# Kernel optimization log

Measured on AMD Instinct MI355X. Metric: run time of the kernel, lower is better.

The kernel has to match this reference:

```python
import jax, jax.numpy as jnp
import numpy as np

DIM = 1024
N_HEAD = 16
HEAD_DIM = DIM // N_HEAD
SCALE = HEAD_DIM ** (-0.5)


def setup_inputs() -> dict:
    key = jax.random.key(0)
    ks = jax.random.split(key, 5)
    x = jax.random.normal(ks[0], (2, 2048, DIM), dtype=jnp.float32)
    # Linear params (torch nn.Linear stores weight as [out, in]; we keep [in, out])
    wqkv = jax.random.normal(ks[1], (DIM, 3 * DIM), dtype=jnp.float32) / np.sqrt(DIM)
    bqkv = jax.random.normal(ks[2], (3 * DIM,), dtype=jnp.float32) * 0.01
    wo = jax.random.normal(ks[3], (DIM, DIM), dtype=jnp.float32) / np.sqrt(DIM)
    bo = jax.random.normal(ks[4], (DIM,), dtype=jnp.float32) * 0.01
    return {"x": x, "wqkv": wqkv, "bqkv": bqkv, "wo": wo, "bo": bo}


def reference(x, wqkv, bqkv, wo, bo):
    b, s, _ = x.shape
    qkv = x @ wqkv + bqkv                      # [b, s, 3*dim]
    q, k, v = jnp.split(qkv, 3, axis=-1)
    # [b, s, h, d] -> [b, h, s, d]
    def heads(t):
        return t.reshape(b, s, N_HEAD, HEAD_DIM).transpose(0, 2, 1, 3)
    q, k, v = heads(q) * SCALE, heads(k), heads(v)
    attn = jnp.einsum('bhqd,bhkd->bhqk', q, k)  # [b, h, s, s]
    attn = jax.nn.softmax(attn, axis=-1)
    out = jnp.einsum('bhqk,bhkd->bhqd', attn, v)
    out = out.transpose(0, 2, 1, 3).reshape(b, s, DIM)
    return out @ wo + bo
```

## Files before the change

### kernel.cpp

```cpp
#include <hip/hip_runtime.h>
#include <hip/hip_bf16.h>

#define DIM   1024
#define NHEAD 16
#define HDIM  64
#define BATCH 2
#define SEQ   2048
#define TOK   (BATCH*SEQ)
#define QSCALE 0.1803368801111204f

typedef unsigned short u16;
typedef __attribute__((ext_vector_type(8))) _Float16 h16x8;
typedef __attribute__((ext_vector_type(2))) __fp16 fp16x2;
typedef __attribute__((ext_vector_type(4))) float f32x4;
typedef __attribute__((ext_vector_type(16))) float f32x16;
typedef __attribute__((ext_vector_type(2))) int i32x2;

__device__ __forceinline__ u16 f2h(float f) {
    union { _Float16 h; u16 u; } v; v.h = (_Float16)f;
    return v.u;
}
__device__ __forceinline__ unsigned pack2h(float a, float b) {
    return (unsigned)f2h(a) | ((unsigned)f2h(b) << 16);
}
__device__ __forceinline__ unsigned pkrtz(float a, float b) {
    union { fp16x2 h; unsigned u; } v;
    v.h = __builtin_amdgcn_cvt_pkrtz(a, b);
    return v.u;
}
__device__ __forceinline__ f32x16 zero16() {
    f32x16 v;
#pragma unroll
    for (int i = 0; i < 16; ++i) v[i] = 0.f;
    return v;
}

typedef __attribute__((address_space(3))) void lds_void;
typedef const __attribute__((address_space(1))) void gbl_void;
__device__ __forceinline__ void gload_lds16(const void* g, void* l) {
    __builtin_amdgcn_global_load_lds((gbl_void*)g, (lds_void*)l, 16, 0, 0);
}

__global__ __launch_bounds__(256)
void cvt_f16(const float* __restrict__ in, u16* __restrict__ out) {
    int i = blockIdx.x * 256 + threadIdx.x;
    float4 v = ((const float4*)in)[i];
    ((uint2*)out)[i] = make_uint2(pack2h(v.x, v.y), pack2h(v.z, v.w));
}

__global__ __launch_bounds__(256)
void cvt_f16_T(const float* __restrict__ in, u16* __restrict__ outT,
               int K, int N) {
    __shared__ float t[32][33];
    const int n0 = blockIdx.x * 32, k0 = blockIdx.y * 32;
    const int tx = threadIdx.x & 31, ty = threadIdx.x >> 5;
#pragma unroll
    for (int i = 0; i < 4; ++i)
        t[ty + i * 8][tx] = in[(size_t)(k0 + ty + i * 8) * N + n0 + tx];
    __syncthreads();
#pragma unroll
    for (int i = 0; i < 4; ++i)
        outT[(size_t)(n0 + ty + i * 8) * K + k0 + tx] = f2h(t[tx][ty + i * 8]);
}

__global__ __launch_bounds__(256)
void gemm_qkv(const u16* __restrict__ Ag, const u16* __restrict__ Bg,
              const float* __restrict__ bias, u16* __restrict__ Qh,
              u16* __restrict__ Kh, u16* __restrict__ Vh, int K, int N) {
    __shared__ u16 As[128 * 64];
    __shared__ u16 Bs[128 * 64];

    const int tid  = threadIdx.x;
    const int lane = tid & 63;
    const int w    = tid >> 6;
    const int c    = lane & 15;
    const int quad = lane >> 4;
    const int wm   = (w & 1) * 64;
    const int wn   = (w >> 1) * 64;
    const int row0 = blockIdx.y * 128;
    const int col0 = blockIdx.x * 128;
    const int sw   = c & 7;

    f32x4 acc[4][4];
#pragma unroll
    for (int m = 0; m < 4; ++m)
#pragma unroll
        for (int n = 0; n < 4; ++n) acc[m][n] = (f32x4){0.f, 0.f, 0.f, 0.f};

    for (int k0 = 0; k0 < K; k0 += 64) {
        __syncthreads();
#pragma unroll
        for (int i = 0; i < 4; ++i) {
            int idx = tid + i * 256;
            int r = idx >> 3, p = idx & 7;
            int g = p ^ (r & 7);
            gload_lds16(Ag + (size_t)(row0 + r) * K + k0 + g * 8, &As[idx * 8]);
            gload_lds16(Bg + (size_t)(col0 + r) * K + k0 + g * 8, &Bs[idx * 8]);
        }
        __syncthreads();

        h16x8 af[4][2];
#pragma unroll
        for (int m = 0; m < 4; ++m)
#pragma unroll
            for (int kh = 0; kh < 2; ++kh)
                af[m][kh] = *(const h16x8*)&As[(wm + m * 16 + c) * 64 +
                                              ((kh * 4 + quad) ^ sw) * 8];
#pragma unroll
        for (int kh = 0; kh < 2; ++kh)
#pragma unroll
            for (int n = 0; n < 4; ++n) {
                h16x8 bf = *(const h16x8*)&Bs[(wn + n * 16 + c) * 64 +
                                              ((kh * 4 + quad) ^ sw) * 8];
#pragma unroll
                for (int m = 0; m < 4; ++m)
                    acc[m][n] = __builtin_amdgcn_mfma_f32_16x16x32_f16(
                        af[m][kh], bf, acc[m][n], 0, 0, 0);
            }
    }

#pragma unroll
    for (int n = 0; n < 4; ++n) {
        const int col = col0 + wn + n * 16 + c;
        const float bv = bias[col];
        const int h = (col >> 6) & 15, d = col & 63;
#pragma unroll
        for (int m = 0; m < 4; ++m) {
            const int rbase = row0 + wm + m * 16 + quad * 4;
            const int b = rbase >> 11, s0 = rbase & (SEQ - 1);
            const int bh = (b << 4) + h;
            if (col0 < DIM) {
#pragma unroll
                for (int r = 0; r < 4; ++r)
                    Qh[((size_t)bh * SEQ + s0 + r) * 64 + d] =
                        f2h((acc[m][n][r] + bv) * QSCALE);
            } else if (col0 < 2 * DIM) {
#pragma unroll
                for (int r = 0; r < 4; ++r)
                    Kh[((size_t)bh * SEQ + s0 + r) * 64 + d] =
                        f2h(acc[m][n][r] + bv);
            } else {
                uint2 pv = make_uint2(pack2h(acc[m][n][0] + bv, acc[m][n][1] + bv),
                                      pack2h(acc[m][n][2] + bv, acc[m][n][3] + bv));
                *(uint2*)&Vh[((size_t)bh * 64 + d) * SEQ + s0] = pv;
            }
        }
    }
}

__global__ __launch_bounds__(256)
void gemm_out(const u16* __restrict__ Ag, const u16* __restrict__ Bg,
              const float* __restrict__ bias, float* __restrict__ Cout,
              int M, int N, int K) {
    __shared__ u16 As[128 * 64];
    __shared__ u16 Bs[64 * 64];

    const int tid  = threadIdx.x;
    const int lane = tid & 63;
    const int w    = tid >> 6;
    const int c    = lane & 15;
    const int quad = lane >> 4;
    const int wm   = w * 32;
    const int row0 = blockIdx.y * 128;
    const int col0 = blockIdx.x * 64;
    const int sw   = c & 7;

    f32x4 acc[2][4];
#pragma unroll
    for (int m = 0; m < 2; ++m)
#pragma unroll
        for (int n = 0; n < 4; ++n) acc[m][n] = (f32x4){0.f, 0.f, 0.f, 0.f};

    for (int k0 = 0; k0 < K; k0 += 64) {
        __syncthreads();
#pragma unroll
        for (int i = 0; i < 4; ++i) {
            int idx = tid + i * 256;
            int r = idx >> 3, p = idx & 7;
            int g = p ^ (r & 7);
            gload_lds16(Ag + (size_t)(row0 + r) * K + k0 + g * 8, &As[idx * 8]);
        }
#pragma unroll
        for (int i = 0; i < 2; ++i) {
            int idx = tid + i * 256;
            int r = idx >> 3, p = idx & 7;
            int g = p ^ (r & 7);
            gload_lds16(Bg + (size_t)(col0 + r) * K + k0 + g * 8, &Bs[idx * 8]);
        }
        __syncthreads();

        h16x8 af[2][2];
#pragma unroll
        for (int m = 0; m < 2; ++m)
#pragma unroll
            for (int kh = 0; kh < 2; ++kh)
                af[m][kh] = *(const h16x8*)&As[(wm + m * 16 + c) * 64 +
                                              ((kh * 4 + quad) ^ sw) * 8];
#pragma unroll
        for (int kh = 0; kh < 2; ++kh)
#pragma unroll
            for (int n = 0; n < 4; ++n) {
                h16x8 bf = *(const h16x8*)&Bs[(n * 16 + c) * 64 +
                                              ((kh * 4 + quad) ^ sw) * 8];
#pragma unroll
                for (int m = 0; m < 2; ++m)
                    acc[m][n] = __builtin_amdgcn_mfma_f32_16x16x32_f16(
                        af[m][kh], bf, acc[m][n], 0, 0, 0);
            }
    }

#pragma unroll
    for (int n = 0; n < 4; ++n) {
        const int col = col0 + n * 16 + c;
        const float bv = bias[col];
#pragma unroll
        for (int m = 0; m < 2; ++m) {
            const int rbase = row0 + wm + m * 16 + quad * 4;
#pragma unroll
            for (int r = 0; r < 4; ++r)
                Cout[(size_t)(rbase + r) * N + col] = acc[m][n][r] + bv;
        }
    }
}

__global__ __launch_bounds__(256, 2)
void flash_attn11(const u16* __restrict__ Qg, const u16* __restrict__ Kg,
                  const u16* __restrict__ Vg, u16* __restrict__ aout) {
    __shared__ u16 Qs[128 * 64];
    __shared__ u16 Ks[2][128 * 64];
    __shared__ u16 Vt[2][64 * 128];

    const int tid  = threadIdx.x;
    const int lane = tid & 63;
    const int w    = tid >> 6;
    const int wq   = w & 1;
    const int wk   = w >> 1;
    const int n32  = lane & 31;
    const int q5   = lane >> 5;
    const int bh   = blockIdx.y;
    const int q0   = blockIdx.x * 128;

    const u16* Qb = Qg + (size_t)bh * SEQ * 64;
    const u16* Kb = Kg + (size_t)bh * SEQ * 64;
    const u16* Vb = Vg + (size_t)bh * 64 * SEQ;

#pragma unroll
    for (int i = 0; i < 4; ++i) {
        int idx = tid + i * 256;
        int r = idx >> 3, p = idx & 7, g = p ^ (r & 7);
        gload_lds16(Qb + (size_t)(q0 + r) * 64 + g * 8, &Qs[idx * 8]);
    }
#pragma unroll
    for (int i = 0; i < 4; ++i) {
        int idx = tid + i * 256;
        int rk = idx >> 3, pk = idx & 7, gk = pk ^ (rk & 7);
        gload_lds16(Kb + (size_t)rk * 64 + gk * 8, &Ks[0][idx * 8]);
        int rv = idx >> 4, cv = idx & 15, gv = cv ^ (rv & 7);
        gload_lds16(Vb + (size_t)rv * SEQ + gv * 8, &Vt[0][idx * 8]);
    }
    __syncthreads();

    const int qrowA = wq * 64 + n32;
    const int qrowB = qrowA + 32;
    const int sw    = n32 & 7;
    h16x8 qbA[4], qbB[4];
#pragma unroll
    for (int s = 0; s < 4; ++s) {
        const int ch = ((s * 2 + q5) ^ sw) * 8;
        qbA[s] = *(const h16x8*)&Qs[qrowA * 64 + ch];
        qbB[s] = *(const h16x8*)&Qs[qrowB * 64 + ch];
    }

    float lA = 0.f, lB = 0.f;
    f32x16 oA[2] = {zero16(), zero16()};
    f32x16 oB[2] = {zero16(), zero16()};

    for (int kt = 0; kt < SEQ / 128; ++kt) {
        const int cur = kt & 1, nxt = cur ^ 1;

        if (kt < SEQ / 128 - 1) {
            const int k1 = (kt + 1) * 128;
#pragma unroll
            for (int i = 0; i < 4; ++i) {
                int idx = tid + i * 256;
                int rk = idx >> 3, pk = idx & 7, gk = pk ^ (rk & 7);
                gload_lds16(Kb + (size_t)(k1 + rk) * 64 + gk * 8, &Ks[nxt][idx * 8]);
                int rv = idx >> 4, cv = idx & 15, gv = cv ^ (rv & 7);
                gload_lds16(Vb + (size_t)rv * SEQ + k1 + gv * 8, &Vt[nxt][idx * 8]);
            }
        }

        unsigned xwA[8][2], xwB[8][2];
#pragma unroll
        for (int sub = 0; sub < 2; ++sub) {
            const int kr = wk * 64 + sub * 32 + n32;
            f32x16 saA = zero16(), saB = zero16();
            __builtin_amdgcn_s_setprio(1);
#pragma unroll
            for (int s = 0; s < 4; ++s) {
                h16x8 ak = *(const h16x8*)&Ks[cur][kr * 64 +
                                                   (((s * 2 + q5) ^ sw) * 8)];
                saA = __builtin_amdgcn_mfma_f32_32x32x16_f16(ak, qbA[s], saA, 0, 0, 0);
                saB = __builtin_amdgcn_mfma_f32_32x32x16_f16(ak, qbB[s], saB, 0, 0, 0);
            }
            __builtin_amdgcn_s_setprio(0);
#pragma unroll
            for (int rr = 0; rr < 4; ++rr) {
                float a0 = __builtin_amdgcn_exp2f(saA[4 * rr + 0]);
                float a1 = __builtin_amdgcn_exp2f(saA[4 * rr + 1]);
                float a2 = __builtin_amdgcn_exp2f(saA[4 * rr + 2]);
                float a3 = __builtin_amdgcn_exp2f(saA[4 * rr + 3]);
                lA += (a0 + a1) + (a2 + a3);
                xwA[sub * 4 + rr][0] = pkrtz(a0, a1);
                xwA[sub * 4 + rr][1] = pkrtz(a2, a3);
                float b0 = __builtin_amdgcn_exp2f(saB[4 * rr + 0]);
                float b1 = __builtin_amdgcn_exp2f(saB[4 * rr + 1]);
                float b2 = __builtin_amdgcn_exp2f(saB[4 * rr + 2]);
                float b3 = __builtin_amdgcn_exp2f(saB[4 * rr + 3]);
                lB += (b0 + b1) + (b2 + b3);
                xwB[sub * 4 + rr][0] = pkrtz(b0, b1);
                xwB[sub * 4 + rr][1] = pkrtz(b2, b3);
            }
        }

        h16x8 bpA[4], bpB[4];
#pragma unroll
        for (int s = 0; s < 4; ++s) {
            i32x2 ra = __builtin_amdgcn_permlane32_swap(
                (int)xwA[2 * s][0], (int)xwA[2 * s + 1][0], false, false);
            i32x2 rb = __builtin_amdgcn_permlane32_swap(
                (int)xwA[2 * s][1], (int)xwA[2 * s + 1][1], false, false);
            union { int u[4]; h16x8 h; } fa;
            fa.u[0] = ra[0]; fa.u[1] = rb[0]; fa.u[2] = ra[1]; fa.u[3] = rb[1];
            bpA[s] = fa.h;
            i32x2 rc = __builtin_amdgcn_permlane32_swap(
                (int)xwB[2 * s][0], (int)xwB[2 * s + 1][0], false, false);
            i32x2 rd = __builtin_amdgcn_permlane32_swap(
                (int)xwB[2 * s][1], (int)xwB[2 * s + 1][1], false, false);
            union { int u[4]; h16x8 h; } fb;
            fb.u[0] = rc[0]; fb.u[1] = rd[0]; fb.u[2] = rc[1]; fb.u[3] = rd[1];
            bpB[s] = fb.h;
        }

        __builtin_amdgcn_s_setprio(1);
#pragma unroll
        for (int dt = 0; dt < 2; ++dt) {
            const int dr = dt * 32 + n32;
#pragma unroll
            for (int s = 0; s < 4; ++s) {
                h16x8 av = *(const h16x8*)&Vt[cur][dr * 128 +
                                                   ((wk * 8 + ((s * 2 + q5) ^ sw)) * 8)];
                oA[dt] = __builtin_amdgcn_mfma_f32_32x32x16_f16(av, bpA[s], oA[dt], 0, 0, 0);
                oB[dt] = __builtin_amdgcn_mfma_f32_32x32x16_f16(av, bpB[s], oB[dt], 0, 0, 0);
            }
        }
        __builtin_amdgcn_s_setprio(0);

        __syncthreads();
    }

    lA += __shfl_xor(lA, 32, 64);
    lB += __shfl_xor(lB, 32, 64);

    float* oc = (float*)Vt;
    float* lc = (float*)Qs;
    const int rowA = (wq * 2 + 0) * 64 + lane;
    const int rowB = (wq * 2 + 1) * 64 + lane;
    if (wk == 1) {
#pragma unroll
        for (int dt = 0; dt < 2; ++dt)
#pragma unroll
            for (int i = 0; i < 16; ++i) {
                oc[rowA * 32 + ((dt * 16 + i + lane) & 31)] = oA[dt][i];
                oc[rowB * 32 + ((dt * 16 + i + lane) & 31)] = oB[dt][i];
            }
        lc[rowA] = lA;
        lc[rowB] = lB;
    }
    __syncthreads();
    if (wk == 1) return;
    lA += lc[rowA];
    lB += lc[rowB];
#pragma unroll
    for (int dt = 0; dt < 2; ++dt)
#pragma unroll
        for (int i = 0; i < 16; ++i) {
            oA[dt][i] += oc[rowA * 32 + ((dt * 16 + i + lane) & 31)];
            oB[dt][i] += oc[rowB * 32 + ((dt * 16 + i + lane) & 31)];
        }

    const float invA = 1.f / lA, invB = 1.f / lB;
    const int b = bh >> 4, h = bh & 15;
    const size_t roA = (size_t)(b * SEQ + q0 + qrowA) * DIM + h * HDIM;
    const size_t roB = (size_t)(b * SEQ + q0 + qrowB) * DIM + h * HDIM;
#pragma unroll
    for (int dt = 0; dt < 2; ++dt) {
#pragma unroll
        for (int rq = 0; rq < 4; ++rq) {
            const int d = dt * 32 + 8 * rq + 4 * q5;
            *(uint2*)&aout[roA + d] = make_uint2(
                pkrtz(oA[dt][4 * rq + 0] * invA, oA[dt][4 * rq + 1] * invA),
                pkrtz(oA[dt][4 * rq + 2] * invA, oA[dt][4 * rq + 3] * invA));
            *(uint2*)&aout[roB + d] = make_uint2(
                pkrtz(oB[dt][4 * rq + 0] * invB, oB[dt][4 * rq + 1] * invB),
                pkrtz(oB[dt][4 * rq + 2] * invB, oB[dt][4 * rq + 3] * invB));
        }
    }
}

extern "C" void kernel_launch(void* const* d_in, const int* in_sizes, int n_in,
                              void* d_out, int out_size, void* d_ws, size_t ws_size,
                              hipStream_t stream) {
    (void)in_sizes; (void)n_in; (void)out_size; (void)ws_size;
    const float* x    = (const float*)d_in[0];
    const float* wqkv = (const float*)d_in[1];
    const float* bqkv = (const float*)d_in[2];
    const float* wo   = (const float*)d_in[3];
    const float* bo   = (const float*)d_in[4];
    float* out = (float*)d_out;

    const size_t HB = (size_t)BATCH * NHEAD * SEQ * HDIM;
    u16* Qh  = (u16*)d_ws;
    u16* Kh  = Qh + HB;
    u16* Vh  = Kh + HB;
    u16* ao  = Vh + HB;
    u16* wqT = ao + (size_t)TOK * DIM;
    u16* woT = wqT + (size_t)3 * DIM * DIM;
    u16* xh  = woT + (size_t)DIM * DIM;

    cvt_f16<<<TOK * DIM / 4 / 256, 256, 0, stream>>>(x, xh);
    cvt_f16_T<<<dim3(3 * DIM / 32, DIM / 32), 256, 0, stream>>>(wqkv, wqT, DIM, 3 * DIM);
    cvt_f16_T<<<dim3(DIM / 32, DIM / 32), 256, 0, stream>>>(wo, woT, DIM, DIM);
    gemm_qkv<<<dim3(3 * DIM / 128, TOK / 128), 256, 0, stream>>>(
        xh, wqT, bqkv, Qh, Kh, Vh, DIM, 3 * DIM);
    flash_attn11<<<dim3(SEQ / 128, BATCH * NHEAD), 256, 0, stream>>>(
        Qh, Kh, Vh, ao);
    gemm_out<<<dim3(DIM / 64, TOK / 128), 256, 0, stream>>>(
        ao, woT, bo, out, TOK, DIM, DIM);
}
```

Measured before the change: 184.8 us.

## Load attention Q/K/V fragments directly from global into registers, drop LDS staging

The attention kernel stops staging Q, K and V tiles in shared memory with double-buffered async copies and block barriers. Each wave now loads its MFMA operand fragments straight from global memory into registers, software-pipelining K one tile ahead, while V is loaded at the start of each iteration. This removes the per-tile __syncthreads and the LDS traffic, but each pair of waves now fetches the same K/V data separately through cache, and uses more registers and longer exposed global latency.

```diff
diff --git a/kernel.cpp b/kernel.cpp
--- a/kernel.cpp
+++ b/kernel.cpp
@@ -224,11 +224,10 @@
 }
 
 __global__ __launch_bounds__(256, 2)
-void flash_attn11(const u16* __restrict__ Qg, const u16* __restrict__ Kg,
+void flash_attn12(const u16* __restrict__ Qg, const u16* __restrict__ Kg,
                   const u16* __restrict__ Vg, u16* __restrict__ aout) {
-    __shared__ u16 Qs[128 * 64];
-    __shared__ u16 Ks[2][128 * 64];
-    __shared__ u16 Vt[2][64 * 128];
+    __shared__ float oc[256 * 32];
+    __shared__ float lc[256];
 
     const int tid  = threadIdx.x;
     const int lane = tid & 63;
@@ -244,64 +243,71 @@
     const u16* Kb = Kg + (size_t)bh * SEQ * 64;
     const u16* Vb = Vg + (size_t)bh * 64 * SEQ;
 
-#pragma unroll
-    for (int i = 0; i < 4; ++i) {
-        int idx = tid + i * 256;
-        int r = idx >> 3, p = idx & 7, g = p ^ (r & 7);
-        gload_lds16(Qb + (size_t)(q0 + r) * 64 + g * 8, &Qs[idx * 8]);
-    }
-#pragma unroll
-    for (int i = 0; i < 4; ++i) {
-        int idx = tid + i * 256;
-        int rk = idx >> 3, pk = idx & 7, gk = pk ^ (rk & 7);
-        gload_lds16(Kb + (size_t)rk * 64 + gk * 8, &Ks[0][idx * 8]);
-        int rv = idx >> 4, cv = idx & 15, gv = cv ^ (rv & 7);
-        gload_lds16(Vb + (size_t)rv * SEQ + gv * 8, &Vt[0][idx * 8]);
-    }
-    __syncthreads();
-
     const int qrowA = wq * 64 + n32;
     const int qrowB = qrowA + 32;
-    const int sw    = n32 & 7;
+    const int ch0 = (0 + q5) * 8, ch1 = (2 + q5) * 8,
+              ch2 = (4 + q5) * 8, ch3 = (6 + q5) * 8;
+
     h16x8 qbA[4], qbB[4];
-#pragma unroll
-    for (int s = 0; s < 4; ++s) {
-        const int ch = ((s * 2 + q5) ^ sw) * 8;
-        qbA[s] = *(const h16x8*)&Qs[qrowA * 64 + ch];
-        qbB[s] = *(const h16x8*)&Qs[qrowB * 64 + ch];
+    {
+        const u16* qa = Qb + (size_t)(q0 + qrowA) * 64;
+        const u16* qb_ = Qb + (size_t)(q0 + qrowB) * 64;
+        qbA[0] = *(const h16x8*)&qa[ch0];  qbA[1] = *(const h16x8*)&qa[ch1];
+        qbA[2] = *(const h16x8*)&qa[ch2];  qbA[3] = *(const h16x8*)&qa[ch3];
+        qbB[0] = *(const h16x8*)&qb_[ch0]; qbB[1] = *(const h16x8*)&qb_[ch1];
+        qbB[2] = *(const h16x8*)&qb_[ch2]; qbB[3] = *(const h16x8*)&qb_[ch3];
     }
 
     float lA = 0.f, lB = 0.f;
     f32x16 oA[2] = {zero16(), zero16()};
     f32x16 oB[2] = {zero16(), zero16()};
 
-    for (int kt = 0; kt < SEQ / 128; ++kt) {
-        const int cur = kt & 1, nxt = cur ^ 1;
-
-        if (kt < SEQ / 128 - 1) {
-            const int k1 = (kt + 1) * 128;
-#pragma unroll
-            for (int i = 0; i < 4; ++i) {
-                int idx = tid + i * 256;
-                int rk = idx >> 3, pk = idx & 7, gk = pk ^ (rk & 7);
-                gload_lds16(Kb + (size_t)(k1 + rk) * 64 + gk * 8, &Ks[nxt][idx * 8]);
-                int rv = idx >> 4, cv = idx & 15, gv = cv ^ (rv & 7);
-                gload_lds16(Vb + (size_t)rv * SEQ + k1 + gv * 8, &Vt[nxt][idx * 8]);
-            }
+    h16x8 kf0[2][4], kf1[2][4];
+    const u16* kr0 = Kb + (size_t)(wk * 64 + n32) * 64;
+    const u16* kr1 = Kb + (size_t)(wk * 64 + 32 + n32) * 64;
+    const u16* vr0 = Vb + (size_t)n32 * SEQ + wk * 64;
+    const u16* vr1 = Vb + (size_t)(32 + n32) * SEQ + wk * 64;
+
+#define LOAD_K(DST, OFF)                                                     \
+    {                                                                        \
+        DST[0][0] = *(const h16x8*)&kr0[(OFF) + ch0];                        \
+        DST[0][1] = *(const h16x8*)&kr0[(OFF) + ch1];                        \
+        DST[0][2] = *(const h16x8*)&kr0[(OFF) + ch2];                        \
+        DST[0][3] = *(const h16x8*)&kr0[(OFF) + ch3];                        \
+        DST[1][0] = *(const h16x8*)&kr1[(OFF) + ch0];                        \
+        DST[1][1] = *(const h16x8*)&kr1[(OFF) + ch1];                        \
+        DST[1][2] = *(const h16x8*)&kr1[(OFF) + ch2];                        \
+        DST[1][3] = *(const h16x8*)&kr1[(OFF) + ch3];                        \
+    }
+
+    LOAD_K(kf0, 0);
+
+    auto iter = [&](h16x8 (&KF)[2][4], h16x8 (&KN)[2][4], int T) {
+        if (T + 1 < SEQ / 128)
+            LOAD_K(KN, (size_t)(T + 1) * 128 * 64);
+
+        h16x8 vf[2][4];
+        {
+            const size_t vo = (size_t)T * 128;
+            vf[0][0] = *(const h16x8*)&vr0[vo + ch0];
+            vf[0][1] = *(const h16x8*)&vr0[vo + ch1];
+            vf[0][2] = *(const h16x8*)&vr0[vo + ch2];
+            vf[0][3] = *(const h16x8*)&vr0[vo + ch3];
+            vf[1][0] = *(const h16x8*)&vr1[vo + ch0];
+            vf[1][1] = *(const h16x8*)&vr1[vo + ch1];
+            vf[1][2] = *(const h16x8*)&vr1[vo + ch2];
+            vf[1][3] = *(const h16x8*)&vr1[vo + ch3];
         }
 
         unsigned xwA[8][2], xwB[8][2];
 #pragma unroll
         for (int sub = 0; sub < 2; ++sub) {
-            const int kr = wk * 64 + sub * 32 + n32;
             f32x16 saA = zero16(), saB = zero16();
             __builtin_amdgcn_s_setprio(1);
 #pragma unroll
             for (int s = 0; s < 4; ++s) {
-                h16x8 ak = *(const h16x8*)&Ks[cur][kr * 64 +
-                                                   (((s * 2 + q5) ^ sw) * 8)];
-                saA = __builtin_amdgcn_mfma_f32_32x32x16_f16(ak, qbA[s], saA, 0, 0, 0);
-                saB = __builtin_amdgcn_mfma_f32_32x32x16_f16(ak, qbB[s], saB, 0, 0, 0);
+                saA = __builtin_amdgcn_mfma_f32_32x32x16_f16(KF[sub][s], qbA[s], saA, 0, 0, 0);
+                saB = __builtin_amdgcn_mfma_f32_32x32x16_f16(KF[sub][s], qbB[s], saB, 0, 0, 0);
             }
             __builtin_amdgcn_s_setprio(0);
 #pragma unroll
@@ -344,26 +350,24 @@
 
         __builtin_amdgcn_s_setprio(1);
 #pragma unroll
-        for (int dt = 0; dt < 2; ++dt) {
-            const int dr = dt * 32 + n32;
+        for (int dt = 0; dt < 2; ++dt)
 #pragma unroll
             for (int s = 0; s < 4; ++s) {
-                h16x8 av = *(const h16x8*)&Vt[cur][dr * 128 +
-                                                   ((wk * 8 + ((s * 2 + q5) ^ sw)) * 8)];
-                oA[dt] = __builtin_amdgcn_mfma_f32_32x32x16_f16(av, bpA[s], oA[dt], 0, 0, 0);
-                oB[dt] = __builtin_amdgcn_mfma_f32_32x32x16_f16(av, bpB[s], oB[dt], 0, 0, 0);
-            }
-        }
+                oA[dt] = __builtin_amdgcn_mfma_f32_32x32x16_f16(vf[dt][s], bpA[s], oA[dt], 0, 0, 0);
+                oB[dt] = __builtin_amdgcn_mfma_f32_32x32x16_f16(vf[dt][s], bpB[s], oB[dt], 0, 0, 0);
+            }
         __builtin_amdgcn_s_setprio(0);
-
-        __syncthreads();
-    }
+    };
+
+    for (int kt = 0; kt < SEQ / 128; kt += 2) {
+        iter(kf0, kf1, kt);
+        iter(kf1, kf0, kt + 1);
+    }
+#undef LOAD_K
 
     lA += __shfl_xor(lA, 32, 64);
     lB += __shfl_xor(lB, 32, 64);
 
-    float* oc = (float*)Vt;
-    float* lc = (float*)Qs;
     const int rowA = (wq * 2 + 0) * 64 + lane;
     const int rowB = (wq * 2 + 1) * 64 + lane;
     if (wk == 1) {
@@ -433,7 +437,7 @@
     cvt_f16_T<<<dim3(DIM / 32, DIM / 32), 256, 0, stream>>>(wo, woT, DIM, DIM);
     gemm_qkv<<<dim3(3 * DIM / 128, TOK / 128), 256, 0, stream>>>(
         xh, wqT, bqkv, Qh, Kh, Vh, DIM, 3 * DIM);
-    flash_attn11<<<dim3(SEQ / 128, BATCH * NHEAD), 256, 0, stream>>>(
+    flash_attn12<<<dim3(SEQ / 128, BATCH * NHEAD), 256, 0, stream>>>(
         Qh, Kh, Vh, ao);
     gemm_out<<<dim3(DIM / 64, TOK / 128), 256, 0, stream>>>(
         ao, woT, bo, out, TOK, DIM, DIM);
```

Result: slower. 249.8 us (+35.2%).

## Double-buffer LDS in both GEMMs and enlarge out-projection tile to 128x128

Applied to the files above, without the earlier changes.

Both projection GEMMs now stage the next K-slice into a second LDS buffer while computing on the current one, which removes one barrier per iteration and overlaps the global-to-LDS loads with MFMA work. The output GEMM also moves from a 128x64 tile to 128x128 with a 2x2 warp layout, giving more reuse per block but half as many blocks (256) on the GPU. Shared memory per block doubles to 64KB, which may lower occupancy. Correctness depends on the async LDS loads being complete at the end-of-iteration barrier.

```diff
diff --git a/kernel.cpp b/kernel.cpp
--- a/kernel.cpp
+++ b/kernel.cpp
@@ -67,8 +67,8 @@
 void gemm_qkv(const u16* __restrict__ Ag, const u16* __restrict__ Bg,
               const float* __restrict__ bias, u16* __restrict__ Qh,
               u16* __restrict__ Kh, u16* __restrict__ Vh, int K, int N) {
-    __shared__ u16 As[128 * 64];
-    __shared__ u16 Bs[128 * 64];
+    __shared__ u16 As[2][128 * 64];
+    __shared__ u16 Bs[2][128 * 64];
 
     const int tid  = threadIdx.x;
     const int lane = tid & 63;
@@ -81,42 +81,50 @@
     const int col0 = blockIdx.x * 128;
     const int sw   = c & 7;
 
-    f32x4 acc[4][4];
-#pragma unroll
-    for (int m = 0; m < 4; ++m)
-#pragma unroll
-        for (int n = 0; n < 4; ++n) acc[m][n] = (f32x4){0.f, 0.f, 0.f, 0.f};
-
-    for (int k0 = 0; k0 < K; k0 += 64) {
-        __syncthreads();
+    auto stage = [&](int buf, int koff) {
 #pragma unroll
         for (int i = 0; i < 4; ++i) {
             int idx = tid + i * 256;
             int r = idx >> 3, p = idx & 7;
             int g = p ^ (r & 7);
-            gload_lds16(Ag + (size_t)(row0 + r) * K + k0 + g * 8, &As[idx * 8]);
-            gload_lds16(Bg + (size_t)(col0 + r) * K + k0 + g * 8, &Bs[idx * 8]);
-        }
-        __syncthreads();
+            gload_lds16(Ag + (size_t)(row0 + r) * K + koff + g * 8, &As[buf][idx * 8]);
+            gload_lds16(Bg + (size_t)(col0 + r) * K + koff + g * 8, &Bs[buf][idx * 8]);
+        }
+    };
+
+    f32x4 acc[4][4];
+#pragma unroll
+    for (int m = 0; m < 4; ++m)
+#pragma unroll
+        for (int n = 0; n < 4; ++n) acc[m][n] = (f32x4){0.f, 0.f, 0.f, 0.f};
+
+    stage(0, 0);
+    __syncthreads();
+    int cur = 0;
+    for (int k0 = 0; k0 < K; k0 += 64) {
+        if (k0 + 64 < K) stage(cur ^ 1, k0 + 64);
 
         h16x8 af[4][2];
 #pragma unroll
         for (int m = 0; m < 4; ++m)
 #pragma unroll
             for (int kh = 0; kh < 2; ++kh)
-                af[m][kh] = *(const h16x8*)&As[(wm + m * 16 + c) * 64 +
-                                              ((kh * 4 + quad) ^ sw) * 8];
+                af[m][kh] = *(const h16x8*)&As[cur][(wm + m * 16 + c) * 64 +
+                                                   ((kh * 4 + quad) ^ sw) * 8];
 #pragma unroll
         for (int kh = 0; kh < 2; ++kh)
 #pragma unroll
             for (int n = 0; n < 4; ++n) {
-                h16x8 bf = *(const h16x8*)&Bs[(wn + n * 16 + c) * 64 +
-                                              ((kh * 4 + quad) ^ sw) * 8];
+                h16x8 bf = *(const h16x8*)&Bs[cur][(wn + n * 16 + c) * 64 +
+                                                   ((kh * 4 + quad) ^ sw) * 8];
 #pragma unroll
                 for (int m = 0; m < 4; ++m)
                     acc[m][n] = __builtin_amdgcn_mfma_f32_16x16x32_f16(
                         af[m][kh], bf, acc[m][n], 0, 0, 0);
             }
+
+        __syncthreads();
+        cur ^= 1;
     }
 
 #pragma unroll
@@ -152,69 +160,72 @@
 void gemm_out(const u16* __restrict__ Ag, const u16* __restrict__ Bg,
               const float* __restrict__ bias, float* __restrict__ Cout,
               int M, int N, int K) {
-    __shared__ u16 As[128 * 64];
-    __shared__ u16 Bs[64 * 64];
+    __shared__ u16 As[2][128 * 64];
+    __shared__ u16 Bs[2][128 * 64];
 
     const int tid  = threadIdx.x;
     const int lane = tid & 63;
     const int w    = tid >> 6;
     const int c    = lane & 15;
     const int quad = lane >> 4;
-    const int wm   = w * 32;
+    const int wm   = (w & 1) * 64;
+    const int wn   = (w >> 1) * 64;
     const int row0 = blockIdx.y * 128;
-    const int col0 = blockIdx.x * 64;
+    const int col0 = blockIdx.x * 128;
     const int sw   = c & 7;
 
-    f32x4 acc[2][4];
-#pragma unroll
-    for (int m = 0; m < 2; ++m)
-#pragma unroll
-        for (int n = 0; n < 4; ++n) acc[m][n] = (f32x4){0.f, 0.f, 0.f, 0.f};
-
-    for (int k0 = 0; k0 < K; k0 += 64) {
-        __syncthreads();
+    auto stage = [&](int buf, int koff) {
 #pragma unroll
         for (int i = 0; i < 4; ++i) {
             int idx = tid + i * 256;
             int r = idx >> 3, p = idx & 7;
             int g = p ^ (r & 7);
-            gload_lds16(Ag + (size_t)(row0 + r) * K + k0 + g * 8, &As[idx * 8]);
-        }
-#pragma unroll
-        for (int i = 0; i < 2; ++i) {
-            int idx = tid + i * 256;
-            int r = idx >> 3, p = idx & 7;
-            int g = p ^ (r & 7);
-            gload_lds16(Bg + (size_t)(col0 + r) * K + k0 + g * 8, &Bs[idx * 8]);
-        }
-        __syncthreads();
-
-        h16x8 af[2][2];
-#pragma unroll
-        for (int m = 0; m < 2; ++m)
+            gload_lds16(Ag + (size_t)(row0 + r) * K + koff + g * 8, &As[buf][idx * 8]);
+            gload_lds16(Bg + (size_t)(col0 + r) * K + koff + g * 8, &Bs[buf][idx * 8]);
+        }
+    };
+
+    f32x4 acc[4][4];
+#pragma unroll
+    for (int m = 0; m < 4; ++m)
+#pragma unroll
+        for (int n = 0; n < 4; ++n) acc[m][n] = (f32x4){0.f, 0.f, 0.f, 0.f};
+
+    stage(0, 0);
+    __syncthreads();
+    int cur = 0;
+    for (int k0 = 0; k0 < K; k0 += 64) {
+        if (k0 + 64 < K) stage(cur ^ 1, k0 + 64);
+
+        h16x8 af[4][2];
+#pragma unroll
+        for (int m = 0; m < 4; ++m)
 #pragma unroll
             for (int kh = 0; kh < 2; ++kh)
-                af[m][kh] = *(const h16x8*)&As[(wm + m * 16 + c) * 64 +
-                                              ((kh * 4 + quad) ^ sw) * 8];
+                af[m][kh] = *(const h16x8*)&As[cur][(wm + m * 16 + c) * 64 +
+                                                   ((kh * 4 + quad) ^ sw) * 8];
 #pragma unroll
         for (int kh = 0; kh < 2; ++kh)
 #pragma unroll
             for (int n = 0; n < 4; ++n) {
-                h16x8 bf = *(const h16x8*)&Bs[(n * 16 + c) * 64 +
-                                              ((kh * 4 + quad) ^ sw) * 8];
-#pragma unroll
-                for (int m = 0; m < 2; ++m)
+                h16x8 bf = *(const h16x8*)&Bs[cur][(wn + n * 16 + c) * 64 +
+                                                   ((kh * 4 + quad) ^ sw) * 8];
+#pragma unroll
+                for (int m = 0; m < 4; ++m)
                     acc[m][n] = __builtin_amdgcn_mfma_f32_16x16x32_f16(
                         af[m][kh], bf, acc[m][n], 0, 0, 0);
             }
+
+        __syncthreads();
+        cur ^= 1;
     }
 
 #pragma unroll
     for (int n = 0; n < 4; ++n) {
-        const int col = col0 + n * 16 + c;
+        const int col = col0 + wn + n * 16 + c;
         const float bv = bias[col];
 #pragma unroll
-        for (int m = 0; m < 2; ++m) {
+        for (int m = 0; m < 4; ++m) {
             const int rbase = row0 + wm + m * 16 + quad * 4;
 #pragma unroll
             for (int r = 0; r < 4; ++r)
@@ -435,6 +446,6 @@
         xh, wqT, bqkv, Qh, Kh, Vh, DIM, 3 * DIM);
     flash_attn11<<<dim3(SEQ / 128, BATCH * NHEAD), 256, 0, stream>>>(
         Qh, Kh, Vh, ao);
-    gemm_out<<<dim3(DIM / 64, TOK / 128), 256, 0, stream>>>(
+    gemm_out<<<dim3(DIM / 128, TOK / 128), 256, 0, stream>>>(
         ao, woT, bo, out, TOK, DIM, DIM);
 }
```

Measured after the change: 190.9 us. 1.03x slower.

## Fuse conversion kernels into one launch and enlarge output GEMM tile to 128x128

Applied to the files above, without the earlier changes.

Merges the x fp16 conversion and the two weight transpose-conversion kernels into one launch, choosing the branch from the block index. This removes two kernel launches and the gaps between them. Also widens the output projection GEMM tile from 128x64 to 128x128, with each wave computing a 64x64 sub-tile, which gives more operand reuse per LDS load. The cost is that the output grid halves to 256 blocks and each thread keeps more accumulator registers, which can lower occupancy.

```diff
diff --git a/kernel.cpp b/kernel.cpp
--- a/kernel.cpp
+++ b/kernel.cpp
@@ -42,17 +42,22 @@
 }
 
 __global__ __launch_bounds__(256)
-void cvt_f16(const float* __restrict__ in, u16* __restrict__ out) {
-    int i = blockIdx.x * 256 + threadIdx.x;
-    float4 v = ((const float4*)in)[i];
-    ((uint2*)out)[i] = make_uint2(pack2h(v.x, v.y), pack2h(v.z, v.w));
-}
-
-__global__ __launch_bounds__(256)
-void cvt_f16_T(const float* __restrict__ in, u16* __restrict__ outT,
-               int K, int N) {
+void fused_cvt(const float* __restrict__ x,    u16* __restrict__ xh,
+               const float* __restrict__ wqkv, u16* __restrict__ wqT,
+               const float* __restrict__ wo,   u16* __restrict__ woT) {
     __shared__ float t[32][33];
-    const int n0 = blockIdx.x * 32, k0 = blockIdx.y * 32;
+    const int bid = blockIdx.x;
+    if (bid < 4096) {
+        int i = bid * 256 + threadIdx.x;
+        float4 v = ((const float4*)x)[i];
+        ((uint2*)xh)[i] = make_uint2(pack2h(v.x, v.y), pack2h(v.z, v.w));
+        return;
+    }
+    const float* in; u16* outT; int K, N, tb;
+    if (bid < 7168) { in = wqkv; outT = wqT; K = 1024; N = 3072; tb = bid - 4096; }
+    else            { in = wo;   outT = woT; K = 1024; N = 1024; tb = bid - 7168; }
+    const int nbx = N / 32;
+    const int n0 = (tb % nbx) * 32, k0 = (tb / nbx) * 32;
     const int tx = threadIdx.x & 31, ty = threadIdx.x >> 5;
 #pragma unroll
     for (int i = 0; i < 4; ++i)
@@ -153,21 +158,22 @@
               const float* __restrict__ bias, float* __restrict__ Cout,
               int M, int N, int K) {
     __shared__ u16 As[128 * 64];
-    __shared__ u16 Bs[64 * 64];
+    __shared__ u16 Bs[128 * 64];
 
     const int tid  = threadIdx.x;
     const int lane = tid & 63;
     const int w    = tid >> 6;
     const int c    = lane & 15;
     const int quad = lane >> 4;
-    const int wm   = w * 32;
+    const int wm   = (w & 1) * 64;
+    const int wn   = (w >> 1) * 64;
     const int row0 = blockIdx.y * 128;
-    const int col0 = blockIdx.x * 64;
+    const int col0 = blockIdx.x * 128;
     const int sw   = c & 7;
 
-    f32x4 acc[2][4];
-#pragma unroll
-    for (int m = 0; m < 2; ++m)
+    f32x4 acc[4][4];
+#pragma unroll
+    for (int m = 0; m < 4; ++m)
 #pragma unroll
         for (int n = 0; n < 4; ++n) acc[m][n] = (f32x4){0.f, 0.f, 0.f, 0.f};
 
@@ -179,19 +185,13 @@
             int r = idx >> 3, p = idx & 7;
             int g = p ^ (r & 7);
             gload_lds16(Ag + (size_t)(row0 + r) * K + k0 + g * 8, &As[idx * 8]);
-        }
-#pragma unroll
-        for (int i = 0; i < 2; ++i) {
-            int idx = tid + i * 256;
-            int r = idx >> 3, p = idx & 7;
-            int g = p ^ (r & 7);
             gload_lds16(Bg + (size_t)(col0 + r) * K + k0 + g * 8, &Bs[idx * 8]);
         }
         __syncthreads();
 
-        h16x8 af[2][2];
-#pragma unroll
-        for (int m = 0; m < 2; ++m)
+        h16x8 af[4][2];
+#pragma unroll
+        for (int m = 0; m < 4; ++m)
 #pragma unroll
             for (int kh = 0; kh < 2; ++kh)
                 af[m][kh] = *(const h16x8*)&As[(wm + m * 16 + c) * 64 +
@@ -200,10 +200,10 @@
         for (int kh = 0; kh < 2; ++kh)
 #pragma unroll
             for (int n = 0; n < 4; ++n) {
-                h16x8 bf = *(const h16x8*)&Bs[(n * 16 + c) * 64 +
+                h16x8 bf = *(const h16x8*)&Bs[(wn + n * 16 + c) * 64 +
                                               ((kh * 4 + quad) ^ sw) * 8];
 #pragma unroll
-                for (int m = 0; m < 2; ++m)
+                for (int m = 0; m < 4; ++m)
                     acc[m][n] = __builtin_amdgcn_mfma_f32_16x16x32_f16(
                         af[m][kh], bf, acc[m][n], 0, 0, 0);
             }
@@ -211,10 +211,10 @@
 
 #pragma unroll
     for (int n = 0; n < 4; ++n) {
-        const int col = col0 + n * 16 + c;
+        const int col = col0 + wn + n * 16 + c;
         const float bv = bias[col];
 #pragma unroll
-        for (int m = 0; m < 2; ++m) {
+        for (int m = 0; m < 4; ++m) {
             const int rbase = row0 + wm + m * 16 + quad * 4;
 #pragma unroll
             for (int r = 0; r < 4; ++r)
@@ -428,13 +428,11 @@
     u16* woT = wqT + (size_t)3 * DIM * DIM;
     u16* xh  = woT + (size_t)DIM * DIM;
 
-    cvt_f16<<<TOK * DIM / 4 / 256, 256, 0, stream>>>(x, xh);
-    cvt_f16_T<<<dim3(3 * DIM / 32, DIM / 32), 256, 0, stream>>>(wqkv, wqT, DIM, 3 * DIM);
-    cvt_f16_T<<<dim3(DIM / 32, DIM / 32), 256, 0, stream>>>(wo, woT, DIM, DIM);
+    fused_cvt<<<8192, 256, 0, stream>>>(x, xh, wqkv, wqT, wo, woT);
     gemm_qkv<<<dim3(3 * DIM / 128, TOK / 128), 256, 0, stream>>>(
         xh, wqT, bqkv, Qh, Kh, Vh, DIM, 3 * DIM);
     flash_attn11<<<dim3(SEQ / 128, BATCH * NHEAD), 256, 0, stream>>>(
         Qh, Kh, Vh, ao);
-    gemm_out<<<dim3(DIM / 64, TOK / 128), 256, 0, stream>>>(
+    gemm_out<<<dim3(DIM / 128, TOK / 128), 256, 0, stream>>>(
         ao, woT, bo, out, TOK, DIM, DIM);
 }
```

Result: no change. 185.3 us (+0.3%).
